# Performance work log

Measured on AMD Instinct MI355X. Metric: run time of the kernel, lower is better.

Reference implementation:

```python
import jax, jax.numpy as jnp
import numpy as np

K = 16  # neighbors per patchlet (init default)


def _gather(points, idx):
    # points: (b, n, c), idx: (b, m, k) -> (b, m, k, c)  (per-batch gather, = utils.index_points)
    return jax.vmap(lambda p, i: p[i])(points, idx)


def setup_inputs() -> dict:
    key = jax.random.key(0)
    point_seq = jax.random.normal(key, (8, 32, 1024, 3), dtype=jnp.float32)  # (b, t, n, 3)
    return {"point_seq": point_seq}


def reference(point_seq):
    b, t, n, d = point_seq.shape
    k = K
    # feat_seq is None in this config -> features are the points themselves
    feat_seq = point_seq
    # feat_seq_2 = cat([feat[:, [0]], feat], 1)[:, :-1]  (previous frame's feats, first frame repeated)
    feat_prev_seq = jnp.concatenate([feat_seq[:, :1], feat_seq[:, :-1]], axis=1)

    # scan over time: carry = tracked centroids x_current (b, n, 3)
    xs = (jnp.swapaxes(point_seq, 0, 1), jnp.swapaxes(feat_prev_seq, 0, 1))  # (t, b, n, .)
    x0 = point_seq[:, 0]  # x2[:, 0]

    def step(x_cur, inp):
        x_next, feat_prev = inp  # (b, n, 3), (b, n, 3)
        # brute-force squared-distance kNN (== keops Kmin_argKmin, ascending)
        q2 = jnp.sum(x_cur * x_cur, axis=-1)[:, :, None]      # (b, n, 1)
        p2 = jnp.sum(x_next * x_next, axis=-1)[:, None, :]    # (b, 1, n)
        d2 = q2 + p2 - 2.0 * jnp.einsum('bqd,bpd->bqp', x_cur, x_next)  # (b, n, n)
        neg_d, idxs = jax.lax.top_k(-d2, k)                   # smallest-k, ascending
        dist = -neg_d                                          # (b, n, k)
        pts = _gather(x_next, idxs)                            # (b, n, k, 3)
        feats = _gather(feat_prev, idxs)                       # (b, n, k, 3)
        x_new = pts[:, :, 0, :]                                # sample_mode == 'nn'
        return x_new, (dist, idxs, pts, feats, x_new)

    _, (dist, idxs, pts, feats, outx) = jax.lax.scan(step, x0, xs)

    # (t, b, ...) -> (b, t, ...)
    dist = jnp.swapaxes(dist, 0, 1)
    idxs = jnp.swapaxes(idxs, 0, 1)
    pts = jnp.swapaxes(pts, 0, 1)          # patchlet_points (b, t, n, k, 3)
    feats = jnp.swapaxes(feats, 0, 1)      # (b, t, n, k, 3)
    outx = jnp.swapaxes(outx, 0, 1)        # x_current (b, t, n, 3)

    # normalize by first-frame anchor point (detached in torch)
    anchor = jax.lax.stop_gradient(pts[:, :1, :, :1, :])  # (b, 1, n, 1, 3)
    normalized = pts - anchor
    patchlet_feats = jnp.concatenate([feats, normalized], axis=-1)  # (b, t, n, k, 6)

    # (idx, distances, patchlets, patchlet_points, patchlet_feats, normalized_patchlet_points, x_current)
    return (idxs, dist, idxs, pts, patchlet_feats, normalized, outx)
```

## Files before the change

kernel.cpp:

```cpp
#include <hip/hip_runtime.h>
#include <stdint.h>

#define NB 8
#define NT 32
#define NN 1024
#define KSEL 16

typedef unsigned long long u64;
typedef unsigned int u32;

#define O_IDX0 0ull
#define O_DIST 4194304ull
#define O_IDX1 8388608ull
#define O_PTS  12582912ull
#define O_PF   25165824ull
#define O_NORM 50331648ull
#define O_OUTX 62914560ull

#define F32_INF __uint_as_float(0x7F800000u)

#if __has_builtin(__builtin_amdgcn_fmed3f)
#define MED3(X, A, B) __builtin_amdgcn_fmed3f((X), (A), (B))
#else
#define MED3(X, A, B) __builtin_fminf(__builtin_fmaxf((X), (A)), (B))
#endif

__device__ __forceinline__ u32 fmap(float f) {
    u32 b = __float_as_uint(f);
    u32 m = (u32)((int)b >> 31) | 0x80000000u;
    return b ^ m;
}
__device__ __forceinline__ float sq3(float x, float y, float z) {
    return __fmaf_rn(z, z, __fmaf_rn(x, x, __fmul_rn(y, y)));
}
__device__ __forceinline__ float d2f(float qx, float qy, float qz, float q2, float4 c) {
    float dot = __fmul_rn(qx, c.x);
    dot = __fmaf_rn(qy, c.y, dot);
    dot = __fmaf_rn(qz, c.z, dot);
    return __fsub_rn(__fadd_rn(q2, c.w), __fadd_rn(dot, dot));
}

#define INSERT16(D2V, JV)                                                        \
{                                                                                \
    _Pragma("unroll")                                                            \
    for (int s = KSEL - 1; s >= 1; --s) {                                        \
        ID[s] = ((D2V) < K[s - 1]) ? ID[s - 1] : (((D2V) < K[s]) ? (JV) : ID[s]);\
        K[s]  = MED3((D2V), K[s - 1], K[s]);                                     \
    }                                                                            \
    ID[0] = ((D2V) < K[0]) ? (JV) : ID[0];                                       \
    K[0]  = __builtin_fminf((D2V), K[0]);                                        \
}

__global__ __launch_bounds__(256) void chain_k(const float* __restrict__ P,
                                               float* __restrict__ outx) {
    __shared__ float4 sF[NN];
    const int tid = threadIdx.x;
    const int bid = blockIdx.x;
    const int b = bid >> 7;
    const int qb = (bid & 127) << 3;
    const int ln = tid & 63;
    const int q = qb + ((tid >> 6) << 1) + (ln >> 5);
    const int sl = ln & 31;
    const float* bp = P + (size_t)b * NT * NN * 3;

    float cx = bp[q * 3 + 0], cy = bp[q * 3 + 1], cz = bp[q * 3 + 2];

    for (int t = 0; t < NT; ++t) {
        const float4* f4 = (const float4*)(bp + (size_t)t * NN * 3);
        float4 A = f4[tid * 3 + 0], Bv = f4[tid * 3 + 1], C = f4[tid * 3 + 2];
        sF[tid * 4 + 0] = make_float4(A.x, A.y, A.z, sq3(A.x, A.y, A.z));
        sF[tid * 4 + 1] = make_float4(A.w, Bv.x, Bv.y, sq3(A.w, Bv.x, Bv.y));
        sF[tid * 4 + 2] = make_float4(Bv.z, Bv.w, C.x, sq3(Bv.z, Bv.w, C.x));
        sF[tid * 4 + 3] = make_float4(C.y, C.z, C.w, sq3(C.y, C.z, C.w));
        __syncthreads();

        float q2 = sq3(cx, cy, cz);
        float bd = F32_INF;
        u32 bj = 0u;
        #pragma unroll 8
        for (int i = 0; i < 32; ++i) {
            int j = (i << 5) | sl;
            float d2 = d2f(cx, cy, cz, q2, sF[j]);
            bool c_ = d2 < bd;
            bd = c_ ? d2 : bd;
            bj = c_ ? (u32)j : bj;
        }
        u64 key = ((u64)fmap(bd) << 32) | (u64)bj;
        #pragma unroll
        for (int off = 1; off < 32; off <<= 1) {
            u64 o = __shfl_xor(key, off);
            key = (o < key) ? o : key;
        }
        int bi = (int)((u32)key & 1023u);
        float4 w = sF[bi];
        cx = w.x; cy = w.y; cz = w.z;
        if (sl == 0) {
            float* o = outx + ((size_t)(b * NT + t) * NN + q) * 3;
            o[0] = cx; o[1] = cy; o[2] = cz;
        }
        __syncthreads();
    }
}

__global__ __launch_bounds__(256, 4) void topk_k(const float* __restrict__ P,
                                                 const float* __restrict__ outx,
                                                 float* __restrict__ out) {
    __shared__ float4 sC[NN];
    __shared__ float4 sPv[NN];
    const int tid = threadIdx.x;
    const int bid = blockIdx.x;
    const int b = bid >> 7;
    const int t = (bid >> 2) & 31;
    const int qc = bid & 3;
    const int q = (qc << 8) | tid;
    const float* bp = P + (size_t)b * NT * NN * 3;

    {
        const float4* f4 = (const float4*)(bp + (size_t)t * NN * 3);
        float4 A = f4[tid * 3 + 0], Bv = f4[tid * 3 + 1], C = f4[tid * 3 + 2];
        sC[tid * 4 + 0] = make_float4(A.x, A.y, A.z, sq3(A.x, A.y, A.z));
        sC[tid * 4 + 1] = make_float4(A.w, Bv.x, Bv.y, sq3(A.w, Bv.x, Bv.y));
        sC[tid * 4 + 2] = make_float4(Bv.z, Bv.w, C.x, sq3(Bv.z, Bv.w, C.x));
        sC[tid * 4 + 3] = make_float4(C.y, C.z, C.w, sq3(C.y, C.z, C.w));
        int tp = (t == 0) ? 0 : (t - 1);
        const float4* g4 = (const float4*)(bp + (size_t)tp * NN * 3);
        A = g4[tid * 3 + 0]; Bv = g4[tid * 3 + 1]; C = g4[tid * 3 + 2];
        sPv[tid * 4 + 0] = make_float4(A.x, A.y, A.z, 0.f);
        sPv[tid * 4 + 1] = make_float4(A.w, Bv.x, Bv.y, 0.f);
        sPv[tid * 4 + 2] = make_float4(Bv.z, Bv.w, C.x, 0.f);
        sPv[tid * 4 + 3] = make_float4(C.y, C.z, C.w, 0.f);
    }
    __syncthreads();

    float cx, cy, cz;
    if (t == 0) {
        const float* qp = bp + (size_t)q * 3;
        cx = qp[0]; cy = qp[1]; cz = qp[2];
    } else {
        const float* qp = outx + ((size_t)(b * NT + (t - 1)) * NN + q) * 3;
        cx = qp[0]; cy = qp[1]; cz = qp[2];
    }
    const float* ap = outx + ((size_t)(b * NT) * NN + q) * 3;
    float ax = ap[0], ay = ap[1], az = ap[2];

    float q2 = sq3(cx, cy, cz);
    float K[KSEL];
    u32 ID[KSEL];
    #pragma unroll
    for (int i = 0; i < KSEL; i++) { K[i] = F32_INF; ID[i] = 0u; }

    for (u32 j = 0; j < 64; ++j) {
        float d2 = d2f(cx, cy, cz, q2, sC[j]);
        INSERT16(d2, j)
    }
    float thr = K[KSEL - 1];

    for (int ch = 1; ch < 16; ++ch) {
        u32 mlo = 0u, mhi = 0u;
        #pragma unroll
        for (int jj = 0; jj < 64; ++jj) {
            float d2 = d2f(cx, cy, cz, q2, sC[(ch << 6) | jj]);
            bool h = d2 < thr;
            if (jj < 32) mlo |= h ? (1u << jj) : 0u;
            else         mhi |= h ? (1u << (jj - 32)) : 0u;
        }
        u64 msk = ((u64)mhi << 32) | (u64)mlo;
        int cm = __builtin_popcountll(msk);
        #pragma unroll
        for (int off = 1; off < 64; off <<= 1) {
            int o = __shfl_xor(cm, off);
            cm = (o > cm) ? o : cm;
        }
        cm = __builtin_amdgcn_readfirstlane(cm);
        for (int i = 0; i < cm; ++i) {
            bool act = msk != 0ull;
            u64 mm = act ? msk : 1ull;
            u32 jj = (u32)__builtin_ctzll(mm);
            msk &= (msk - 1ull);
            u32 j = ((u32)ch << 6) | jj;
            float4 c = sC[j];
            float d2 = d2f(cx, cy, cz, q2, c);
            float d2v = act ? d2 : F32_INF;
            INSERT16(d2v, j)
        }
        thr = K[KSEL - 1];
    }

    size_t g = (size_t)(b * NT + t) * NN + q;

    #pragma unroll
    for (int kk = 0; kk < KSEL; kk += 4) {
        float4 fi = make_float4((float)ID[kk + 0], (float)ID[kk + 1],
                                (float)ID[kk + 2], (float)ID[kk + 3]);
        float4 fd = make_float4(K[kk + 0], K[kk + 1], K[kk + 2], K[kk + 3]);
        *(float4*)(out + O_IDX0 + g * 16 + kk) = fi;
        *(float4*)(out + O_IDX1 + g * 16 + kk) = fi;
        *(float4*)(out + O_DIST + g * 16 + kk) = fd;
    }

    #pragma unroll
    for (int kk = 0; kk < KSEL; kk += 4) {
        u32 i0 = ID[kk + 0], i1 = ID[kk + 1], i2 = ID[kk + 2], i3 = ID[kk + 3];
        float4 p0 = sC[i0], p1 = sC[i1], p2v = sC[i2], p3 = sC[i3];
        float4 f0 = sPv[i0], f1 = sPv[i1], f2v = sPv[i2], f3 = sPv[i3];
        float n0x = p0.x - ax, n0y = p0.y - ay, n0z = p0.z - az;
        float n1x = p1.x - ax, n1y = p1.y - ay, n1z = p1.z - az;
        float n2x = p2v.x - ax, n2y = p2v.y - ay, n2z = p2v.z - az;
        float n3x = p3.x - ax, n3y = p3.y - ay, n3z = p3.z - az;

        float* pp = out + O_PTS + g * 48 + kk * 3;
        ((float4*)pp)[0] = make_float4(p0.x, p0.y, p0.z, p1.x);
        ((float4*)pp)[1] = make_float4(p1.y, p1.z, p2v.x, p2v.y);
        ((float4*)pp)[2] = make_float4(p2v.z, p3.x, p3.y, p3.z);

        float* np = out + O_NORM + g * 48 + kk * 3;
        ((float4*)np)[0] = make_float4(n0x, n0y, n0z, n1x);
        ((float4*)np)[1] = make_float4(n1y, n1z, n2x, n2y);
        ((float4*)np)[2] = make_float4(n2z, n3x, n3y, n3z);

        float* fp = out + O_PF + g * 96 + kk * 6;
        ((float4*)fp)[0] = make_float4(f0.x, f0.y, f0.z, n0x);
        ((float4*)fp)[1] = make_float4(n0y, n0z, f1.x, f1.y);
        ((float4*)fp)[2] = make_float4(f1.z, n1x, n1y, n1z);
        ((float4*)fp)[3] = make_float4(f2v.x, f2v.y, f2v.z, n2x);
        ((float4*)fp)[4] = make_float4(n2y, n2z, f3.x, f3.y);
        ((float4*)fp)[5] = make_float4(f3.z, n3x, n3y, n3z);
    }
}

extern "C" void kernel_launch(void* const* d_in, const int* in_sizes, int n_in,
                              void* d_out, int out_size, void* d_ws, size_t ws_size,
                              hipStream_t stream) {
    const float* P = (const float*)d_in[0];
    float* out = (float*)d_out;
    float* outx = out + O_OUTX;
    chain_k<<<dim3(1024), dim3(256), 0, stream>>>(P, outx);
    topk_k<<<dim3(1024), dim3(256), 0, stream>>>(P, outx, out);
}
```

Baseline: 378.9 us.

## Halve topk block size and gather previous-frame features from global memory

The top-k kernel now launches 2048 blocks of 128 threads, each covering 128 queries instead of 256. The shared-memory copy of the previous frame's features is removed, and those features are gathered straight from global memory (where they are likely cached). Shared memory per block drops from 32KB to 16KB, which allows more resident blocks and more parallelism. The cost is that each block still loads the full 1024-point frame, so staging work per query doubles, and the feature gathers become scattered global loads.

```diff
diff --git a/kernel.cpp b/kernel.cpp
--- a/kernel.cpp
+++ b/kernel.cpp
@@ -102,33 +102,32 @@
     }
 }
 
-__global__ __launch_bounds__(256, 4) void topk_k(const float* __restrict__ P,
+__global__ __launch_bounds__(128, 4) void topk_k(const float* __restrict__ P,
                                                  const float* __restrict__ outx,
                                                  float* __restrict__ out) {
     __shared__ float4 sC[NN];
-    __shared__ float4 sPv[NN];
     const int tid = threadIdx.x;
     const int bid = blockIdx.x;
-    const int b = bid >> 7;
-    const int t = (bid >> 2) & 31;
-    const int qc = bid & 3;
-    const int q = (qc << 8) | tid;
+    const int b = bid >> 8;
+    const int t = (bid >> 3) & 31;
+    const int qc = bid & 7;
+    const int q = (qc << 7) | tid;
     const float* bp = P + (size_t)b * NT * NN * 3;
+    const int tp = (t == 0) ? 0 : (t - 1);
+    const float* fpv = bp + (size_t)tp * NN * 3;
 
     {
         const float4* f4 = (const float4*)(bp + (size_t)t * NN * 3);
-        float4 A = f4[tid * 3 + 0], Bv = f4[tid * 3 + 1], C = f4[tid * 3 + 2];
-        sC[tid * 4 + 0] = make_float4(A.x, A.y, A.z, sq3(A.x, A.y, A.z));
-        sC[tid * 4 + 1] = make_float4(A.w, Bv.x, Bv.y, sq3(A.w, Bv.x, Bv.y));
-        sC[tid * 4 + 2] = make_float4(Bv.z, Bv.w, C.x, sq3(Bv.z, Bv.w, C.x));
-        sC[tid * 4 + 3] = make_float4(C.y, C.z, C.w, sq3(C.y, C.z, C.w));
-        int tp = (t == 0) ? 0 : (t - 1);
-        const float4* g4 = (const float4*)(bp + (size_t)tp * NN * 3);
-        A = g4[tid * 3 + 0]; Bv = g4[tid * 3 + 1]; C = g4[tid * 3 + 2];
-        sPv[tid * 4 + 0] = make_float4(A.x, A.y, A.z, 0.f);
-        sPv[tid * 4 + 1] = make_float4(A.w, Bv.x, Bv.y, 0.f);
-        sPv[tid * 4 + 2] = make_float4(Bv.z, Bv.w, C.x, 0.f);
-        sPv[tid * 4 + 3] = make_float4(C.y, C.z, C.w, 0.f);
+        float4 A = f4[tid * 6 + 0], B = f4[tid * 6 + 1], C = f4[tid * 6 + 2];
+        sC[tid * 8 + 0] = make_float4(A.x, A.y, A.z, sq3(A.x, A.y, A.z));
+        sC[tid * 8 + 1] = make_float4(A.w, B.x, B.y, sq3(A.w, B.x, B.y));
+        sC[tid * 8 + 2] = make_float4(B.z, B.w, C.x, sq3(B.z, B.w, C.x));
+        sC[tid * 8 + 3] = make_float4(C.y, C.z, C.w, sq3(C.y, C.z, C.w));
+        float4 D = f4[tid * 6 + 3], E = f4[tid * 6 + 4], F = f4[tid * 6 + 5];
+        sC[tid * 8 + 4] = make_float4(D.x, D.y, D.z, sq3(D.x, D.y, D.z));
+        sC[tid * 8 + 5] = make_float4(D.w, E.x, E.y, sq3(D.w, E.x, E.y));
+        sC[tid * 8 + 6] = make_float4(E.z, E.w, F.x, sq3(E.z, E.w, F.x));
+        sC[tid * 8 + 7] = make_float4(F.y, F.z, F.w, sq3(F.y, F.z, F.w));
     }
     __syncthreads();
 
@@ -202,7 +201,10 @@
     for (int kk = 0; kk < KSEL; kk += 4) {
         u32 i0 = ID[kk + 0], i1 = ID[kk + 1], i2 = ID[kk + 2], i3 = ID[kk + 3];
         float4 p0 = sC[i0], p1 = sC[i1], p2v = sC[i2], p3 = sC[i3];
-        float4 f0 = sPv[i0], f1 = sPv[i1], f2v = sPv[i2], f3 = sPv[i3];
+        float f0x = fpv[i0 * 3 + 0], f0y = fpv[i0 * 3 + 1], f0z = fpv[i0 * 3 + 2];
+        float f1x = fpv[i1 * 3 + 0], f1y = fpv[i1 * 3 + 1], f1z = fpv[i1 * 3 + 2];
+        float f2x = fpv[i2 * 3 + 0], f2y = fpv[i2 * 3 + 1], f2z = fpv[i2 * 3 + 2];
+        float f3x = fpv[i3 * 3 + 0], f3y = fpv[i3 * 3 + 1], f3z = fpv[i3 * 3 + 2];
         float n0x = p0.x - ax, n0y = p0.y - ay, n0z = p0.z - az;
         float n1x = p1.x - ax, n1y = p1.y - ay, n1z = p1.z - az;
         float n2x = p2v.x - ax, n2y = p2v.y - ay, n2z = p2v.z - az;
@@ -219,12 +221,12 @@
         ((float4*)np)[2] = make_float4(n2z, n3x, n3y, n3z);
 
         float* fp = out + O_PF + g * 96 + kk * 6;
-        ((float4*)fp)[0] = make_float4(f0.x, f0.y, f0.z, n0x);
-        ((float4*)fp)[1] = make_float4(n0y, n0z, f1.x, f1.y);
-        ((float4*)fp)[2] = make_float4(f1.z, n1x, n1y, n1z);
-        ((float4*)fp)[3] = make_float4(f2v.x, f2v.y, f2v.z, n2x);
-        ((float4*)fp)[4] = make_float4(n2y, n2z, f3.x, f3.y);
-        ((float4*)fp)[5] = make_float4(f3.z, n3x, n3y, n3z);
+        ((float4*)fp)[0] = make_float4(f0x, f0y, f0z, n0x);
+        ((float4*)fp)[1] = make_float4(n0y, n0z, f1x, f1y);
+        ((float4*)fp)[2] = make_float4(f1z, n1x, n1y, n1z);
+        ((float4*)fp)[3] = make_float4(f2x, f2y, f2z, n2x);
+        ((float4*)fp)[4] = make_float4(n2y, n2z, f3x, f3y);
+        ((float4*)fp)[5] = make_float4(f3z, n3x, n3y, n3z);
     }
 }
 
@@ -235,5 +237,5 @@
     float* out = (float*)d_out;
     float* outx = out + O_OUTX;
     chain_k<<<dim3(1024), dim3(256), 0, stream>>>(P, outx);
-    topk_k<<<dim3(1024), dim3(256), 0, stream>>>(P, outx, out);
-}
+    topk_k<<<dim3(2048), dim3(128), 0, stream>>>(P, outx, out);
+}
```

New measurement: 383.6 us. Within noise of the previous version (+1.3%).
